# Optimization experiments

Measured on AMD Instinct MI355X. Metric: run time of the kernel, lower is better.

Reference implementation:

```python
import jax, jax.numpy as jnp
import numpy as np
from jax import lax

B, N, C = 4, 8000, 91
IMG_H, IMG_W = 800, 1333
WX, WY, WW, WH = 10.0, 10.0, 5.0, 5.0
BBOX_XFORM_CLIP = float(np.log(1000.0 / 16.0))
SCORE_THRESH = 0.05
NMS_THRESH = 0.5
DET_PER_IMG = 100
MIN_SIZE = 0.01
NEG = jnp.float32(-1e30)


def setup_inputs() -> dict:
    key = jax.random.key(0)
    k1, k2, k3 = jax.random.split(key, 3)
    class_logits = jax.random.normal(k1, (B * N, C), dtype=jnp.float32) * 2.0
    box_regression = jax.random.normal(k2, (B * N, C * 4), dtype=jnp.float32) * 0.5
    p = jax.random.uniform(k3, (B, N, 4), dtype=jnp.float32)
    x1 = p[..., 0] * (IMG_W - 150.0)
    y1 = p[..., 1] * (IMG_H - 150.0)
    x2 = x1 + 4.0 + p[..., 2] * 140.0
    y2 = y1 + 4.0 + p[..., 3] * 140.0
    proposals = jnp.stack([x1, y1, x2, y2], axis=-1)
    return {"class_logits": class_logits, "box_regression": box_regression, "proposals": proposals}


def _decode(rel, props):
    # torchvision BoxCoder.decode with weights (10,10,5,5). rel: [N, C*4], props: [N, 4]
    w = props[:, 2] - props[:, 0]
    h = props[:, 3] - props[:, 1]
    cx = props[:, 0] + 0.5 * w
    cy = props[:, 1] + 0.5 * h
    rel = rel.reshape(rel.shape[0], -1, 4)  # [N, C, 4]
    dx = rel[..., 0] / WX
    dy = rel[..., 1] / WY
    dw = jnp.minimum(rel[..., 2] / WW, BBOX_XFORM_CLIP)
    dh = jnp.minimum(rel[..., 3] / WH, BBOX_XFORM_CLIP)
    pcx = dx * w[:, None] + cx[:, None]
    pcy = dy * h[:, None] + cy[:, None]
    pw = jnp.exp(dw) * w[:, None]
    ph = jnp.exp(dh) * h[:, None]
    return jnp.stack([pcx - 0.5 * pw, pcy - 0.5 * ph, pcx + 0.5 * pw, pcy + 0.5 * ph], axis=-1)


def _iou_one_vs_all(b, bs):
    # b: [4], bs: [M, 4]
    ix1 = jnp.maximum(b[0], bs[:, 0])
    iy1 = jnp.maximum(b[1], bs[:, 1])
    ix2 = jnp.minimum(b[2], bs[:, 2])
    iy2 = jnp.minimum(b[3], bs[:, 3])
    inter = jnp.clip(ix2 - ix1, 0.0) * jnp.clip(iy2 - iy1, 0.0)
    a1 = (b[2] - b[0]) * (b[3] - b[1])
    a2 = (bs[:, 2] - bs[:, 0]) * (bs[:, 3] - bs[:, 1])
    return inter / (a1 + a2 - inter)


def _process_image(logits, rel, props):
    # logits: [N, C], rel: [N, C*4], props: [N, 4]
    boxes = _decode(rel, props)  # [N, C, 4]
    # clip_boxes_to_image
    boxes = jnp.stack([
        jnp.clip(boxes[..., 0], 0.0, IMG_W),
        jnp.clip(boxes[..., 1], 0.0, IMG_H),
        jnp.clip(boxes[..., 2], 0.0, IMG_W),
        jnp.clip(boxes[..., 3], 0.0, IMG_H),
    ], axis=-1)
    scores = jax.nn.softmax(logits, axis=-1)
    # drop background class 0 and flatten to [N*(C-1)] candidates
    boxes = boxes[:, 1:, :].reshape(-1, 4)
    scores = scores[:, 1:].reshape(-1)
    labels = jnp.broadcast_to(jnp.arange(1, C, dtype=jnp.int32), (N, C - 1)).reshape(-1)
    bw = boxes[:, 2] - boxes[:, 0]
    bh = boxes[:, 3] - boxes[:, 1]
    valid = (scores > SCORE_THRESH) & (bw >= MIN_SIZE) & (bh >= MIN_SIZE)
    # batched_nms: offset boxes per class so cross-class boxes never overlap
    sg_boxes = lax.stop_gradient(boxes)
    sg_scores = lax.stop_gradient(jnp.where(valid, scores, NEG))
    off = labels.astype(boxes.dtype) * (sg_boxes.max() + 1.0)
    nb = sg_boxes + off[:, None]

    def step(s, _):
        i = jnp.argmax(s)
        si = s[i]
        iou = _iou_one_vs_all(nb[i], nb)
        s2 = jnp.where(iou > NMS_THRESH, NEG, s).at[i].set(NEG)
        return s2, (i, si > NEG / 2)

    _, (idxs, ok) = lax.scan(step, sg_scores, None, length=DET_PER_IMG)
    det_boxes = jnp.where(ok[:, None], boxes[idxs], 0.0)
    det_scores = jnp.where(ok, scores[idxs], 0.0)
    det_labels = jnp.where(ok, labels[idxs], 0)
    return det_boxes, det_scores, det_labels


def reference(class_logits, box_regression, proposals):
    logits = class_logits.reshape(B, N, C)
    rel = box_regression.reshape(B, N, C * 4)
    boxes, scores, labels = jax.vmap(_process_image)(logits, rel, proposals)
    return boxes, scores, labels
```

## Files before the change

### kernel.cpp

```cpp
#include <hip/hip_runtime.h>
#include <math.h>

#pragma clang fp contract(off)

#define NB 4
#define NN 8000
#define NC 91
#define CM1 90
#define CAP 2048
#define ACAP 256
#define ATHR 192
#define GCAP 65536
#define RPB 32
#define BPI (NN / RPB)
#define LCAP 608
#define GWB 16
#define MWB 4

#define CNT_W(b) ((b) * 64)
#define MAX_W(b) (256 + (b) * 64)
#define CNTA_W(b) (512 + (b) * 64)
#define CNTR_W(b) (768 + (b) * 64)
#define HIST_OFF 1024
#define ZERO_WORDS (HIST_OFF + NB * 1024)
#define GBOX_OFF 5120
#define GSC_OFF (GBOX_OFF + NB * GCAP * 4)
#define GOID_OFF (GSC_OFF + NB * GCAP)
#define ABOX_OFF (GOID_OFF + NB * GCAP)
#define AKEY_OFF (ABOX_OFF + NB * ACAP * 4)
#define RBOX_OFF (AKEY_OFF + NB * ACAP * 2)
#define RKEY_OFF (RBOX_OFF + NB * CAP * 4)
#define MTX_OFF (RKEY_OFF + NB * CAP * 2)

__global__ void init_kernel(int* ws_i) {
  const int i = blockIdx.x * 256 + threadIdx.x;
  if (i < ZERO_WORDS) ws_i[i] = 0;
}

__global__ void __launch_bounds__(256) cand_kernel(const float* __restrict__ logits,
                                                   const float* __restrict__ rel,
                                                   const float* __restrict__ props,
                                                   int* __restrict__ ws_i,
                                                   float* __restrict__ ws_f) {
  const int blk = blockIdx.x;
  const int b = blk / BPI;
  const int ib = blk - b * BPI;
  const int t = threadIdx.x;
  const int L = t & 15;
  const int grp = t >> 4;
  const int lane = t & 63;

  __shared__ float sbx[LCAP][4];
  __shared__ float ssb[LCAP];
  __shared__ int soidb[LCAP];
  __shared__ int lhist[1024];
  __shared__ int scnt;
  __shared__ int smaxs;
  __shared__ int sgbase;
  for (int j = t; j < 1024; j += 256) lhist[j] = 0;
  if (t == 0) { scnt = 0; smaxs = 0; }
  __syncthreads();

  int tmax = 0;

  for (int i = 0; i < RPB / 16; ++i) {
    const int row = b * NN + ib * RPB + i * 16 + grp;
    const float* lp = logits + (size_t)row * NC;

    float lv[6];
#pragma unroll
    for (int j = 0; j < 6; ++j) {
      const int k = L + 16 * j;
      lv[j] = (k < NC) ? lp[k] : -INFINITY;
    }
    float tm0 = fmax(lv[0], lv[4]), tm1 = fmax(lv[1], lv[5]);
    float tm2 = lv[2], tm3 = lv[3];
    float um0 = fmax(tm0, tm2), um1 = fmax(tm1, tm3);
    float m = fmax(um0, um1);
    m = fmaxf(m, __shfl_xor(m, 8));
    m = fmaxf(m, __shfl_xor(m, 4));
    m = fmaxf(m, __shfl_xor(m, 2));
    m = fmaxf(m, __shfl_xor(m, 1));

    float ev[6];
#pragma unroll
    for (int j = 0; j < 6; ++j) {
      const int k = L + 16 * j;
      ev[j] = (k < NC) ? expf(lv[j] - m) : 0.0f;
    }
    float ts0 = ev[0] + ev[4], ts1 = ev[1] + ev[5];
    float ts2 = ev[2], ts3 = ev[3];
    float us0 = ts0 + ts2, us1 = ts1 + ts3;
    float sum = us0 + us1;
    sum += __shfl_xor(sum, 8);
    sum += __shfl_xor(sum, 4);
    sum += __shfl_xor(sum, 2);
    sum += __shfl_xor(sum, 1);

    const float4 p = reinterpret_cast<const float4*>(props)[row];
    const float w = p.z - p.x, h = p.w - p.y;
    const float cx = p.x + 0.5f * w, cy = p.y + 0.5f * h;

#pragma unroll
    for (int j = 0; j < 6; ++j) {
      const int c = L + 16 * j;
      if (c >= 1 && c < NC) {
        const float4 r = reinterpret_cast<const float4*>(rel)[(size_t)row * NC + c];
        const float dx = r.x / 10.0f, dy = r.y / 10.0f;
        const float dw = fminf(r.z / 5.0f, 4.135166556742356f);
        const float dh = fminf(r.w / 5.0f, 4.135166556742356f);
        const float pcx = dx * w + cx, pcy = dy * h + cy;
        const float pw = expf(dw) * w, ph = expf(dh) * h;
        float x1 = pcx - 0.5f * pw, y1 = pcy - 0.5f * ph;
        float x2 = pcx + 0.5f * pw, y2 = pcy + 0.5f * ph;
        x1 = fminf(fmaxf(x1, 0.0f), 1333.0f);
        y1 = fminf(fmaxf(y1, 0.0f), 800.0f);
        x2 = fminf(fmaxf(x2, 0.0f), 1333.0f);
        y2 = fminf(fmaxf(y2, 0.0f), 800.0f);
        const float score = ev[j] / sum;
        const float localmax = fmaxf(fmaxf(x1, y1), fmaxf(x2, y2));
        tmax = max(tmax, __float_as_int(localmax));
        const float bw = x2 - x1, bh = y2 - y1;
        if ((score > 0.05f) && (bw >= 0.01f) && (bh >= 0.01f)) {
          const int slot = atomicAdd(&scnt, 1);
          sbx[slot][0] = x1; sbx[slot][1] = y1;
          sbx[slot][2] = x2; sbx[slot][3] = y2;
          ssb[slot] = score;
          soidb[slot] = (row - b * NN) * CM1 + (c - 1);
          int bi = (int)(__float_as_uint(score) >> 16) - 15360;
          bi = min(max(bi, 0), 1023);
          atomicAdd(&lhist[bi], 1);
        }
      }
    }
  }
  tmax = max(tmax, __shfl_xor(tmax, 32));
  tmax = max(tmax, __shfl_xor(tmax, 16));
  tmax = max(tmax, __shfl_xor(tmax, 8));
  tmax = max(tmax, __shfl_xor(tmax, 4));
  tmax = max(tmax, __shfl_xor(tmax, 2));
  tmax = max(tmax, __shfl_xor(tmax, 1));
  if (lane == 0) atomicMax(&smaxs, tmax);
  __syncthreads();
  const int n = scnt;
  if (t == 0) {
    sgbase = atomicAdd(&ws_i[CNT_W(b)], n);
    atomicMax(&ws_i[MAX_W(b)], smaxs);
  }
  __syncthreads();
  const int gb = sgbase;
  for (int j = t; j < n; j += 256) {
    const int pos = gb + j;
    if (pos < GCAP) {
      reinterpret_cast<float4*>(ws_f + GBOX_OFF)[b * GCAP + pos] =
          make_float4(sbx[j][0], sbx[j][1], sbx[j][2], sbx[j][3]);
      ws_f[GSC_OFF + b * GCAP + pos] = ssb[j];
      ws_i[GOID_OFF + b * GCAP + pos] = soidb[j];
    }
  }
  for (int j = t; j < 1024; j += 256) {
    const int v = lhist[j];
    if (v) atomicAdd(&ws_i[HIST_OFF + b * 1024 + j], v);
  }
}

__global__ void __launch_bounds__(256) gather_kernel(int* __restrict__ ws_i,
                                                     float* __restrict__ ws_f) {
  const int b = blockIdx.x / GWB, sub = blockIdx.x % GWB;
  const int t = threadIdx.x;
  __shared__ int seg[256];
  __shared__ int best1, best2;
  __shared__ int lidxA[ACAP];
  __shared__ int lidxR[CAP];
  __shared__ int cA, cR, baseA, baseR;

  const int* H = ws_i + HIST_OFF + b * 1024;
  const int h0 = H[4 * t + 0], h1 = H[4 * t + 1];
  const int h2 = H[4 * t + 2], h3 = H[4 * t + 3];
  seg[t] = h0 + h1 + h2 + h3;
  if (t == 0) { best1 = 1024; best2 = 1024; cA = 0; cR = 0; }
  __syncthreads();
  for (int off = 1; off < 256; off <<= 1) {
    const int v = (t + off < 256) ? seg[t + off] : 0;
    __syncthreads();
    seg[t] += v;
    __syncthreads();
  }
  const int higher = (t < 255) ? seg[t + 1] : 0;
  {
    int A = higher; int cnd = 0x7FFFFFFF;
    A += h3; if (A <= CAP) cnd = 4 * t + 3;
    A += h2; if (A <= CAP) cnd = 4 * t + 2;
    A += h1; if (A <= CAP) cnd = 4 * t + 1;
    A += h0; if (A <= CAP) cnd = 4 * t + 0;
    if (cnd != 0x7FFFFFFF) atomicMin(&best1, cnd);
  }
  {
    int A = higher; int cnd = 0x7FFFFFFF;
    A += h3; if (A <= ATHR) cnd = 4 * t + 3;
    A += h2; if (A <= ATHR) cnd = 4 * t + 2;
    A += h1; if (A <= ATHR) cnd = 4 * t + 1;
    A += h0; if (A <= ATHR) cnd = 4 * t + 0;
    if (cnd != 0x7FFFFFFF) atomicMin(&best2, cnd);
  }
  __syncthreads();
  const int tk = best1, tk2 = best2;

  int M = ws_i[CNT_W(b)];
  if (M > GCAP) M = GCAP;
  const float* gsc = ws_f + GSC_OFF + (size_t)b * GCAP;
  const int* goid = ws_i + GOID_OFF + (size_t)b * GCAP;
  const float4* gbox = reinterpret_cast<const float4*>(ws_f + GBOX_OFF) + (size_t)b * GCAP;
  float4* abox = reinterpret_cast<float4*>(ws_f + ABOX_OFF) + (size_t)b * ACAP;
  unsigned long long* akey = reinterpret_cast<unsigned long long*>(ws_i + AKEY_OFF) + (size_t)b * ACAP;
  float4* rbox = reinterpret_cast<float4*>(ws_f + RBOX_OFF) + (size_t)b * CAP;
  unsigned long long* rkey = reinterpret_cast<unsigned long long*>(ws_i + RKEY_OFF) + (size_t)b * CAP;

  for (int j = sub * 256 + t; j < M; j += GWB * 256) {
    const float s = gsc[j];
    int bi = (int)(__float_as_uint(s) >> 16) - 15360;
    bi = min(max(bi, 0), 1023);
    if (bi >= tk2) {
      const int p = atomicAdd(&cA, 1);
      if (p < ACAP) lidxA[p] = j;
    } else if (bi >= tk) {
      const int p = atomicAdd(&cR, 1);
      if (p < CAP) lidxR[p] = j;
    }
  }
  __syncthreads();
  const int nAb = min(cA, ACAP), nRb = min(cR, CAP);
  if (t == 0) {
    baseA = atomicAdd(&ws_i[CNTA_W(b)], nAb);
    baseR = atomicAdd(&ws_i[CNTR_W(b)], nRb);
  }
  __syncthreads();
  for (int k = t; k < nAb; k += 256) {
    const int j = lidxA[k];
    const int pos = baseA + k;
    if (pos < ACAP) {
      abox[pos] = gbox[j];
      akey[pos] = ((unsigned long long)(__float_as_uint(gsc[j]) | 0x80000000u) << 32) |
                  (unsigned)(0xFFFFFFFFu - (unsigned)goid[j]);
    }
  }
  for (int k = t; k < nRb; k += 256) {
    const int j = lidxR[k];
    const int pos = baseR + k;
    if (pos < CAP) {
      rbox[pos] = gbox[j];
      rkey[pos] = ((unsigned long long)(__float_as_uint(gsc[j]) | 0x80000000u) << 32) |
                  (unsigned)(0xFFFFFFFFu - (unsigned)goid[j]);
    }
  }
}

__global__ void __launch_bounds__(256) matrix_kernel(const int* __restrict__ ws_i,
                                                     const float* __restrict__ ws_f,
                                                     int* __restrict__ ws_mtx) {
  const int b = blockIdx.x / MWB, sub = blockIdx.x % MWB;
  const int t = threadIdx.x;
  __shared__ unsigned long long akey[ACAP];
  __shared__ float4 abox[ACAP];
  __shared__ float4 sboxS[ACAP];
  __shared__ int slblS[ACAP];

  const int nA = min(ws_i[CNTA_W(b)], ACAP);
  const float maxp1 = __int_as_float(ws_i[MAX_W(b)]) + 1.0f;
  const float4* gA = reinterpret_cast<const float4*>(ws_f + ABOX_OFF) + (size_t)b * ACAP;
  const unsigned long long* gAk =
      reinterpret_cast<const unsigned long long*>(ws_i + AKEY_OFF) + (size_t)b * ACAP;

  akey[t] = (t < nA) ? gAk[t] : 0ull;
  if (t < nA) abox[t] = gA[t];
  sboxS[t] = make_float4(0.f, 0.f, 0.f, 0.f);
  slblS[t] = -1;
  __syncthreads();
  {
    const unsigned long long kj = akey[t];
    if (kj != 0ull) {
      int rank = 0;
#pragma unroll 16
      for (int i = 0; i < ACAP; ++i) rank += (akey[i] > kj) ? 1 : 0;
      sboxS[rank] = abox[t];
      const unsigned oid = 0xFFFFFFFFu - (unsigned)(kj & 0xFFFFFFFFull);
      slblS[rank] = (int)(oid % 90u) + 1;
    }
  }
  __syncthreads();

  const int i = sub * 64 + (t >> 2);
  const int q = t & 3;
  const int li = slblS[i];
  const float4 bi = sboxS[i];
  const float oi = (float)li * maxp1;
  const float n0 = bi.x + oi, n1 = bi.y + oi;
  const float n2 = bi.z + oi, n3 = bi.w + oi;
  const float a1 = (n2 - n0) * (n3 - n1);
  unsigned long long r = 0;
#pragma unroll 8
  for (int k = 0; k < 64; ++k) {
    const int j = q * 64 + k;
    const int lj = slblS[j];
    const float4 bj = sboxS[j];
    const float q0 = bj.x + oi, q1 = bj.y + oi;
    const float q2 = bj.z + oi, q3 = bj.w + oi;
    const float ix1 = fmaxf(n0, q0), iy1 = fmaxf(n1, q1);
    const float ix2 = fminf(n2, q2), iy2 = fminf(n3, q3);
    const float inter = fmaxf(ix2 - ix1, 0.0f) * fmaxf(iy2 - iy1, 0.0f);
    const float a2 = (q2 - q0) * (q3 - q1);
    const float iou = inter / ((a1 + a2) - inter);
    const bool hit = (j > i) & (lj == li) & (iou > 0.5f);
    r |= hit ? (1ull << k) : 0ull;
  }
  unsigned long long* mtx =
      reinterpret_cast<unsigned long long*>(ws_mtx + MTX_OFF) + (size_t)b * 1024;
  mtx[i * 4 + q] = r;
}

__global__ void __launch_bounds__(256) greedy_kernel(const int* __restrict__ ws_i,
                                                     const float* __restrict__ ws_f,
                                                     float* __restrict__ out) {
  const int b = blockIdx.x;
  const int t = threadIdx.x;
  const int lane = t & 63;
  __shared__ __align__(16) char sm[57344];
  unsigned long long* akey = (unsigned long long*)sm;
  float4* abox = (float4*)(sm + 2048);
  unsigned long long* skeyS = (unsigned long long*)(sm + 6144);
  float4* sboxS = (float4*)(sm + 8192);
  int* slblS = (int*)(sm + 12288);
  unsigned long long* suppm = (unsigned long long*)(sm + 13312);
  unsigned long long* rkeyS = (unsigned long long*)sm;
  float4* rboxS = (float4*)(sm + 16384);
  int* rlblS = (int*)(sm + 49152);
  __shared__ float4 selbox[100];
  __shared__ unsigned long long selkey[100];
  __shared__ int sellbl[100];
  __shared__ int selpos[100];
  __shared__ int s_cnt;
  __shared__ int snacc;

  const int nA = min(ws_i[CNTA_W(b)], ACAP);
  const int nR = min(ws_i[CNTR_W(b)], CAP);
  const float maxp1 = __int_as_float(ws_i[MAX_W(b)]) + 1.0f;
  const float4* gA = reinterpret_cast<const float4*>(ws_f + ABOX_OFF) + (size_t)b * ACAP;
  const unsigned long long* gAk =
      reinterpret_cast<const unsigned long long*>(ws_i + AKEY_OFF) + (size_t)b * ACAP;
  const unsigned long long* mtx =
      reinterpret_cast<const unsigned long long*>(ws_i + MTX_OFF) + (size_t)b * 1024;

  akey[t] = (t < nA) ? gAk[t] : 0ull;
  if (t < nA) abox[t] = gA[t];
  skeyS[t] = 0ull;
  sboxS[t] = make_float4(0.f, 0.f, 0.f, 0.f);
  slblS[t] = -1;
  __syncthreads();
  {
    const unsigned long long kj = akey[t];
    if (kj != 0ull) {
      int rank = 0;
#pragma unroll 16
      for (int i = 0; i < ACAP; ++i) rank += (akey[i] > kj) ? 1 : 0;
      skeyS[rank] = kj;
      sboxS[rank] = abox[t];
      const unsigned oid = 0xFFFFFFFFu - (unsigned)(kj & 0xFFFFFFFFull);
      slblS[rank] = (int)(oid % 90u) + 1;
    }
  }
#pragma unroll
  for (int j2 = 0; j2 < 4; ++j2) suppm[j2 * 256 + t] = mtx[j2 * 256 + t];
  __syncthreads();

  if (t < 64) {
    unsigned long long m0 = 0, m1 = 0, m2 = 0, m3 = 0;
    int cnt = 0;
    int mypos0 = 0, mypos1 = 0;
#define NMS_CHUNK(W, MW)                                                  \
    if (cnt < 100 && (W)*64 < nA) {                                       \
      for (int base = 0; base < 64 && cnt < 100; base += 8) {             \
        unsigned long long sr0[8], sr1[8], sr2[8], sr3[8];                \
        _Pragma("unroll")                                                 \
        for (int k = 0; k < 8; ++k) {                                     \
          const int j = (W) * 64 + base + k;                              \
          sr0[k] = suppm[j * 4 + 0];                                      \
          sr1[k] = suppm[j * 4 + 1];                                      \
          sr2[k] = suppm[j * 4 + 2];                                      \
          sr3[k] = suppm[j * 4 + 3];                                      \
        }                                                                 \
        _Pragma("unroll")                                                 \
        for (int k = 0; k < 8; ++k) {                                     \
          const int j = (W) * 64 + base + k;                              \
          const bool acc =                                                \
              (j < nA) && (cnt < 100) && !((MW >> (base + k)) & 1ull);    \
          if (acc) {                                                      \
            if (cnt == lane) mypos0 = j;                                  \
            if (cnt == 64 + lane) mypos1 = j;                             \
            ++cnt;                                                        \
            m0 |= sr0[k]; m1 |= sr1[k]; m2 |= sr2[k]; m3 |= sr3[k];       \
          }                                                               \
        }                                                                 \
      }                                                                   \
    }
    NMS_CHUNK(0, m0)
    NMS_CHUNK(1, m1)
    NMS_CHUNK(2, m2)
    NMS_CHUNK(3, m3)
#undef NMS_CHUNK
    selpos[lane] = mypos0;
    if (lane < 36) selpos[64 + lane] = mypos1;
    if (lane == 0) s_cnt = cnt;
  }
  __syncthreads();
  const int cnt = s_cnt;

  if (cnt >= 100 || nR == 0) {
    const int nf = min(cnt, 100);
    if (t < 100) {
      float o0 = 0.f, o1 = 0.f, o2 = 0.f, o3 = 0.f, sc = 0.f, lb = 0.f;
      if (t < nf) {
        const int mypos = selpos[t];
        const float4 v = sboxS[mypos];
        o0 = v.x; o1 = v.y; o2 = v.z; o3 = v.w;
        sc = __uint_as_float((unsigned)(skeyS[mypos] >> 32) & 0x7FFFFFFFu);
        lb = (float)slblS[mypos];
      }
      float* ob = out + ((size_t)b * 100 + t) * 4;
      ob[0] = o0; ob[1] = o1; ob[2] = o2; ob[3] = o3;
      out[NB * 100 * 4 + b * 100 + t] = sc;
      out[NB * 100 * 4 + NB * 100 + b * 100 + t] = lb;
    }
    return;
  }

  float A0x = 0.f, A0y = 0.f, A0z = 0.f, A0w = 0.f; int L0 = -1;
  float A1x = 0.f, A1y = 0.f, A1z = 0.f, A1w = 0.f; int L1 = -1;
  int nacc = 0;

  if (t < 64) {
    unsigned long long k0 = skeyS[0], k1 = skeyS[1];
    float4 b0 = sboxS[0], b1 = sboxS[1];
    int l0 = slblS[0], l1 = slblS[1];
    for (int j = 0; j < ACAP; ++j) {
      if (k0 == 0ull) break;
      const int jp = j + 2;
      unsigned long long k2 = 0ull;
      float4 b2 = make_float4(0.f, 0.f, 0.f, 0.f);
      int l2 = 0;
      if (jp < ACAP) { k2 = skeyS[jp]; b2 = sboxS[jp]; l2 = slblS[jp]; }
      const float oi = (float)l0 * maxp1;
      const float q0 = b0.x + oi, q1 = b0.y + oi;
      const float q2 = b0.z + oi, q3 = b0.w + oi;
      const float a2 = (q2 - q0) * (q3 - q1);
      bool sup = false;
      if (L0 == l0) {
        const float n0 = A0x + oi, n1 = A0y + oi, n2 = A0z + oi, n3 = A0w + oi;
        const float a1 = (n2 - n0) * (n3 - n1);
        const float ix1 = fmaxf(n0, q0), iy1 = fmaxf(n1, q1);
        const float ix2 = fminf(n2, q2), iy2 = fminf(n3, q3);
        const float inter = fmaxf(ix2 - ix1, 0.0f) * fmaxf(iy2 - iy1, 0.0f);
        const float iou = inter / ((a1 + a2) - inter);
        sup = (iou > 0.5f);
      }
      if (L1 == l0) {
        const float n0 = A1x + oi, n1 = A1y + oi, n2 = A1z + oi, n3 = A1w + oi;
        const float a1 = (n2 - n0) * (n3 - n1);
        const float ix1 = fmaxf(n0, q0), iy1 = fmaxf(n1, q1);
        const float ix2 = fminf(n2, q2), iy2 = fminf(n3, q3);
        const float inter = fmaxf(ix2 - ix1, 0.0f) * fmaxf(iy2 - iy1, 0.0f);
        const float iou = inter / ((a1 + a2) - inter);
        sup = sup || (iou > 0.5f);
      }
      if (!__any(sup ? 1 : 0)) {
        if (nacc < 64) {
          if (lane == nacc) { A0x = b0.x; A0y = b0.y; A0z = b0.z; A0w = b0.w; L0 = l0; }
        } else {
          if (lane == nacc - 64) { A1x = b0.x; A1y = b0.y; A1z = b0.z; A1w = b0.w; L1 = l0; }
        }
        if (lane == 0) { selbox[nacc] = b0; selkey[nacc] = k0; sellbl[nacc] = l0; }
        ++nacc;
        if (nacc == 100) break;
      }
      k0 = k1; b0 = b1; l0 = l1;
      k1 = k2; b1 = b2; l1 = l2;
    }
    if (lane == 0) snacc = nacc;
  }
  __syncthreads();

  if (snacc < 100 && nR > 0) {
    const float4* gR = reinterpret_cast<const float4*>(ws_f + RBOX_OFF) + (size_t)b * CAP;
    const unsigned long long* gRk =
        reinterpret_cast<const unsigned long long*>(ws_i + RKEY_OFF) + (size_t)b * CAP;
    for (int j = t; j < CAP; j += 256) {
      const unsigned long long k = (j < nR) ? gRk[j] : 0ull;
      rkeyS[j] = k;
      if (j < nR) {
        rboxS[j] = gR[j];
        const unsigned oid = 0xFFFFFFFFu - (unsigned)(k & 0xFFFFFFFFull);
        rlblS[j] = (int)(oid % 90u) + 1;
      }
    }
    __syncthreads();
    if (t < 64) {
      while (nacc < 100) {
        unsigned long long mk = 0ull; int mi = 0;
        for (int j = lane; j < nR; j += 64) {
          const unsigned long long k = rkeyS[j];
          if (k > mk) { mk = k; mi = j; }
        }
        for (int mm = 1; mm < 64; mm <<= 1) {
          const unsigned long long ok = __shfl_xor(mk, mm);
          const int om = __shfl_xor(mi, mm);
          if (ok > mk) { mk = ok; mi = om; }
        }
        if (mk == 0ull) break;
        if (lane == 0) rkeyS[mi] = 0ull;
        __asm__ volatile("s_waitcnt lgkmcnt(0)" ::: "memory");
        const int lbl = rlblS[mi];
        const float4 bb = rboxS[mi];
        const float oi = (float)lbl * maxp1;
        const float q0 = bb.x + oi, q1 = bb.y + oi;
        const float q2 = bb.z + oi, q3 = bb.w + oi;
        const float a2 = (q2 - q0) * (q3 - q1);
        bool sup = false;
        if (L0 == lbl) {
          const float n0 = A0x + oi, n1 = A0y + oi, n2 = A0z + oi, n3 = A0w + oi;
          const float a1 = (n2 - n0) * (n3 - n1);
          const float ix1 = fmaxf(n0, q0), iy1 = fmaxf(n1, q1);
          const float ix2 = fminf(n2, q2), iy2 = fminf(n3, q3);
          const float inter = fmaxf(ix2 - ix1, 0.0f) * fmaxf(iy2 - iy1, 0.0f);
          const float iou = inter / ((a1 + a2) - inter);
          sup = (iou > 0.5f);
        }
        if (L1 == lbl) {
          const float n0 = A1x + oi, n1 = A1y + oi, n2 = A1z + oi, n3 = A1w + oi;
          const float a1 = (n2 - n0) * (n3 - n1);
          const float ix1 = fmaxf(n0, q0), iy1 = fmaxf(n1, q1);
          const float ix2 = fminf(n2, q2), iy2 = fminf(n3, q3);
          const float inter = fmaxf(ix2 - ix1, 0.0f) * fmaxf(iy2 - iy1, 0.0f);
          const float iou = inter / ((a1 + a2) - inter);
          sup = sup || (iou > 0.5f);
        }
        if (!__any(sup ? 1 : 0)) {
          if (nacc < 64) {
            if (lane == nacc) { A0x = bb.x; A0y = bb.y; A0z = bb.z; A0w = bb.w; L0 = lbl; }
          } else {
            if (lane == nacc - 64) { A1x = bb.x; A1y = bb.y; A1z = bb.z; A1w = bb.w; L1 = lbl; }
          }
          if (lane == 0) { selbox[nacc] = bb; selkey[nacc] = mk; sellbl[nacc] = lbl; }
          ++nacc;
        }
      }
      if (lane == 0) snacc = nacc;
    }
    __syncthreads();
  }

  const int nf = snacc;
  for (int k2 = t; k2 < 100; k2 += 256) {
    float o0 = 0.f, o1 = 0.f, o2 = 0.f, o3 = 0.f, sc = 0.f, lb = 0.f;
    if (k2 < nf) {
      const float4 v = selbox[k2];
      o0 = v.x; o1 = v.y; o2 = v.z; o3 = v.w;
      sc = __uint_as_float((unsigned)(selkey[k2] >> 32) & 0x7FFFFFFFu);
      lb = (float)sellbl[k2];
    }
    float* ob = out + ((size_t)b * 100 + k2) * 4;
    ob[0] = o0; ob[1] = o1; ob[2] = o2; ob[3] = o3;
    out[NB * 100 * 4 + b * 100 + k2] = sc;
    out[NB * 100 * 4 + NB * 100 + b * 100 + k2] = lb;
  }
}

extern "C" void kernel_launch(void* const* d_in, const int* in_sizes, int n_in,
                              void* d_out, int out_size, void* d_ws, size_t ws_size,
                              hipStream_t stream) {
  const float* logits = (const float*)d_in[0];
  const float* rel = (const float*)d_in[1];
  const float* props = (const float*)d_in[2];
  float* out = (float*)d_out;
  int* ws_i = (int*)d_ws;
  float* ws_f = (float*)d_ws;

  init_kernel<<<(ZERO_WORDS + 255) / 256, 256, 0, stream>>>(ws_i);
  cand_kernel<<<NB * BPI, 256, 0, stream>>>(logits, rel, props, ws_i, ws_f);
  gather_kernel<<<NB * GWB, 256, 0, stream>>>(ws_i, ws_f);
  matrix_kernel<<<NB * MWB, 256, 0, stream>>>(ws_i, ws_f, ws_i);
  greedy_kernel<<<NB, 256, 0, stream>>>(ws_i, ws_f, out);
}
```

Before: 71.54 us.

## Move score histogram into gather kernel and use wave-aggregated slot allocation

```diff
diff --git a/kernel.cpp b/kernel.cpp
--- a/kernel.cpp
+++ b/kernel.cpp
@@ -21,8 +21,7 @@
 #define MAX_W(b) (256 + (b) * 64)
 #define CNTA_W(b) (512 + (b) * 64)
 #define CNTR_W(b) (768 + (b) * 64)
-#define HIST_OFF 1024
-#define ZERO_WORDS (HIST_OFF + NB * 1024)
+#define ZERO_WORDS 1024
 #define GBOX_OFF 5120
 #define GSC_OFF (GBOX_OFF + NB * GCAP * 4)
 #define GOID_OFF (GSC_OFF + NB * GCAP)
@@ -53,11 +52,9 @@
   __shared__ float sbx[LCAP][4];
   __shared__ float ssb[LCAP];
   __shared__ int soidb[LCAP];
-  __shared__ int lhist[1024];
   __shared__ int scnt;
   __shared__ int smaxs;
   __shared__ int sgbase;
-  for (int j = t; j < 1024; j += 256) lhist[j] = 0;
   if (t == 0) { scnt = 0; smaxs = 0; }
   __syncthreads();
 
@@ -104,6 +101,8 @@
 #pragma unroll
     for (int j = 0; j < 6; ++j) {
       const int c = L + 16 * j;
+      bool valid = false;
+      float x1 = 0.f, y1 = 0.f, x2 = 0.f, y2 = 0.f, score = 0.f;
       if (c >= 1 && c < NC) {
         const float4 r = reinterpret_cast<const float4*>(rel)[(size_t)row * NC + c];
         const float dx = r.x / 10.0f, dy = r.y / 10.0f;
@@ -111,26 +110,30 @@
         const float dh = fminf(r.w / 5.0f, 4.135166556742356f);
         const float pcx = dx * w + cx, pcy = dy * h + cy;
         const float pw = expf(dw) * w, ph = expf(dh) * h;
-        float x1 = pcx - 0.5f * pw, y1 = pcy - 0.5f * ph;
-        float x2 = pcx + 0.5f * pw, y2 = pcy + 0.5f * ph;
+        x1 = pcx - 0.5f * pw; y1 = pcy - 0.5f * ph;
+        x2 = pcx + 0.5f * pw; y2 = pcy + 0.5f * ph;
         x1 = fminf(fmaxf(x1, 0.0f), 1333.0f);
         y1 = fminf(fmaxf(y1, 0.0f), 800.0f);
         x2 = fminf(fmaxf(x2, 0.0f), 1333.0f);
         y2 = fminf(fmaxf(y2, 0.0f), 800.0f);
-        const float score = ev[j] / sum;
+        score = ev[j] / sum;
         const float localmax = fmaxf(fmaxf(x1, y1), fmaxf(x2, y2));
         tmax = max(tmax, __float_as_int(localmax));
         const float bw = x2 - x1, bh = y2 - y1;
-        if ((score > 0.05f) && (bw >= 0.01f) && (bh >= 0.01f)) {
-          const int slot = atomicAdd(&scnt, 1);
-          sbx[slot][0] = x1; sbx[slot][1] = y1;
-          sbx[slot][2] = x2; sbx[slot][3] = y2;
-          ssb[slot] = score;
-          soidb[slot] = (row - b * NN) * CM1 + (c - 1);
-          int bi = (int)(__float_as_uint(score) >> 16) - 15360;
-          bi = min(max(bi, 0), 1023);
-          atomicAdd(&lhist[bi], 1);
-        }
+        valid = (score > 0.05f) && (bw >= 0.01f) && (bh >= 0.01f);
+      }
+      const unsigned long long mk = __ballot(valid);
+      if (valid) {
+        const int leader = __ffsll(mk) - 1;
+        const int rank = __popcll(mk & ((1ull << lane) - 1));
+        int basel = 0;
+        if (lane == leader) basel = atomicAdd(&scnt, __popcll(mk));
+        basel = __shfl(basel, leader);
+        const int slot = basel + rank;
+        sbx[slot][0] = x1; sbx[slot][1] = y1;
+        sbx[slot][2] = x2; sbx[slot][3] = y2;
+        ssb[slot] = score;
+        soidb[slot] = (row - b * NN) * CM1 + (c - 1);
       }
     }
   }
@@ -158,27 +161,36 @@
       ws_i[GOID_OFF + b * GCAP + pos] = soidb[j];
     }
   }
-  for (int j = t; j < 1024; j += 256) {
-    const int v = lhist[j];
-    if (v) atomicAdd(&ws_i[HIST_OFF + b * 1024 + j], v);
-  }
 }
 
 __global__ void __launch_bounds__(256) gather_kernel(int* __restrict__ ws_i,
                                                      float* __restrict__ ws_f) {
   const int b = blockIdx.x / GWB, sub = blockIdx.x % GWB;
   const int t = threadIdx.x;
+  __shared__ int lh[1024];
   __shared__ int seg[256];
   __shared__ int best1, best2;
   __shared__ int lidxA[ACAP];
   __shared__ int lidxR[CAP];
   __shared__ int cA, cR, baseA, baseR;
 
-  const int* H = ws_i + HIST_OFF + b * 1024;
-  const int h0 = H[4 * t + 0], h1 = H[4 * t + 1];
-  const int h2 = H[4 * t + 2], h3 = H[4 * t + 3];
+  int M = ws_i[CNT_W(b)];
+  if (M > GCAP) M = GCAP;
+  const float* gsc = ws_f + GSC_OFF + (size_t)b * GCAP;
+
+  for (int j = t; j < 1024; j += 256) lh[j] = 0;
+  if (t == 0) { best1 = 1024; best2 = 1024; cA = 0; cR = 0; }
+  __syncthreads();
+  for (int j = t; j < M; j += 256) {
+    int bi = (int)(__float_as_uint(gsc[j]) >> 16) - 15360;
+    bi = min(max(bi, 0), 1023);
+    atomicAdd(&lh[bi], 1);
+  }
+  __syncthreads();
+
+  const int h0 = lh[4 * t + 0], h1 = lh[4 * t + 1];
+  const int h2 = lh[4 * t + 2], h3 = lh[4 * t + 3];
   seg[t] = h0 + h1 + h2 + h3;
-  if (t == 0) { best1 = 1024; best2 = 1024; cA = 0; cR = 0; }
   __syncthreads();
   for (int off = 1; off < 256; off <<= 1) {
     const int v = (t + off < 256) ? seg[t + off] : 0;
@@ -206,9 +218,6 @@
   __syncthreads();
   const int tk = best1, tk2 = best2;
 
-  int M = ws_i[CNT_W(b)];
-  if (M > GCAP) M = GCAP;
-  const float* gsc = ws_f + GSC_OFF + (size_t)b * GCAP;
   const int* goid = ws_i + GOID_OFF + (size_t)b * GCAP;
   const float4* gbox = reinterpret_cast<const float4*>(ws_f + GBOX_OFF) + (size_t)b * GCAP;
   float4* abox = reinterpret_cast<float4*>(ws_f + ABOX_OFF) + (size_t)b * ACAP;
```

Result: slower. 99.96 us (+39.7%).
